# Kernel optimization log

Measured on AMD Instinct MI355X. Metric: run time of the kernel, lower is better.

Reference implementation:

```python
import jax, jax.numpy as jnp
import numpy as np

MANIFOLD_DIM = 256
EPS = 1e-8

def quaternion_normalize(q):
    # q: (..., 4) -> unit quaternions
    return q / (jnp.linalg.norm(q, axis=-1, keepdims=True) + EPS)

def quaternion_mul(a, b):
    # Hamilton product, broadcasting over leading dims. a, b: (..., 4)
    aw, ax, ay, az = a[..., 0], a[..., 1], a[..., 2], a[..., 3]
    bw, bx, by, bz = b[..., 0], b[..., 1], b[..., 2], b[..., 3]
    return jnp.stack([
        aw * bw - ax * bx - ay * by - az * bz,
        aw * bx + ax * bw + ay * bz - az * by,
        aw * by - ax * bz + ay * bw + az * bx,
        aw * bz + ax * by - ay * bx + az * bw,
    ], axis=-1)

def compute_berry_phase(path):
    # path: (B, N, 4). gamma = 2*acos(Re(q0*q1*...*q_{N-1}*q0))
    path = quaternion_normalize(path)
    # ordered product via log-depth parallel scan (quaternion mul is associative)
    prod_all = jax.lax.associative_scan(quaternion_mul, path, axis=1)[:, -1]  # (B, 4)
    prod = quaternion_mul(prod_all, path[:, 0])
    return 2.0 * jnp.arccos(jnp.clip(prod[..., 0], -1.0, 1.0))  # (B,)

def holomorphic_audit(q_state):
    # torch.gradient(t)[0] == gradient along dim 0 (batch axis), unit spacing.
    # dw+dx+dy+dz == gradient of the component-sum (linearity of gradient).
    df = jnp.abs(jnp.gradient(q_state.sum(axis=-1), axis=0))  # (B, N)
    res = jnp.mean(df)
    return res < 0.05, res

def _to_quaternion(x):
    B = x.shape[0]
    return x.reshape(B, -1, 4)

def setup_inputs() -> dict:
    key = jax.random.key(0)
    ks = jax.random.split(key, 9)
    B, HW, L, G, D = 8, 4096, 8192, 4096, MANIFOLD_DIM
    s = 0.05  # keep latents small so Berry product stays numerically tame
    return {
        "vision_data": jax.random.normal(ks[0], (B, HW, 3), jnp.float32),
        "text_data": jax.random.normal(ks[1], (B, L, 1), jnp.float32),
        "genomic_data": jax.random.normal(ks[2], (B, G, 4), jnp.float32),
        "Wv": jax.random.normal(ks[3], (3, D), jnp.float32) * s,
        "bv": jax.random.normal(ks[4], (D,), jnp.float32) * s,
        "Wt": jax.random.normal(ks[5], (1, D), jnp.float32) * s,
        "bt": jax.random.normal(ks[6], (D,), jnp.float32) * s,
        "Wg": jax.random.normal(ks[7], (4, D), jnp.float32) * s,
        "bg": jax.random.normal(ks[8], (D,), jnp.float32) * s,
    }

def reference(vision_data, text_data, genomic_data, Wv, bv, Wt, bt, Wg, bg):
    v_lat = vision_data @ Wv + bv      # (B, HW, 256)
    t_lat = text_data @ Wt + bt        # (B, L, 256)
    g_lat = genomic_data @ Wg + bg     # (B, G, 256)
    v_path = _to_quaternion(v_lat)     # (B, HW*64, 4)
    t_path = _to_quaternion(t_lat)
    g_path = _to_quaternion(g_lat)
    phi_v = compute_berry_phase(v_path)
    phi_t = compute_berry_phase(t_path)
    phi_g = compute_berry_phase(g_path)
    interference = jnp.abs(phi_v.mean() - phi_t.mean())
    genomic_invariant_score = jnp.exp(-jnp.abs(phi_g - interference))  # (B,)
    _, res_v = holomorphic_audit(v_path)
    _, res_t = holomorphic_audit(t_path)
    return genomic_invariant_score, interference, res_v, res_t
```

## Files before the change

kernel.cpp:

```cpp
#include <hip/hip_runtime.h>
#include <math.h>

#define BB 8
#define HW 4096
#define LTXT 8192
#define GG 4096
#define DD 256


struct QF { float w, x, y, z; };

__device__ __forceinline__ QF qmulf(const QF a, const QF b) {
    QF r;
    r.w = fmaf(a.w, b.w, -fmaf(a.x, b.x, fmaf(a.y, b.y, a.z * b.z)));
    r.x = fmaf(a.w, b.x, fmaf(a.x, b.w, fmaf(a.y, b.z, -(a.z * b.y))));
    r.y = fmaf(a.w, b.y, fmaf(a.y, b.w, fmaf(a.z, b.x, -(a.x * b.z))));
    r.z = fmaf(a.w, b.z, fmaf(a.x, b.y, fmaf(a.z, b.w, -(a.y * b.x))));
    return r;
}

__device__ __forceinline__ QF wave_ordered_prod(QF p, int lane) {
    #pragma unroll
    for (int s = 1; s < 64; s <<= 1) {
        QF o;
        o.w = __shfl_xor(p.w, s, 64);
        o.x = __shfl_xor(p.x, s, 64);
        o.y = __shfl_xor(p.y, s, 64);
        o.z = __shfl_xor(p.z, s, 64);
        const bool hi = (lane & s) != 0;
        QF a = hi ? o : p;
        QF b = hi ? p : o;
        p = qmulf(a, b);
    }
    return p;
}

template<int K, int BQ>
__device__ __forceinline__ void chain_block(
    const float* __restrict__ X, const float* __restrict__ W,
    const float* __restrict__ bias, int rowBase,
    float* __restrict__ out4, float* sprod)
{
    constexpr int V = K + 1;
    constexpr int NB = 64 / BQ;
    const int t = threadIdx.x;
    const int r = rowBase + t;
    float xv[K];
    #pragma unroll
    for (int k = 0; k < K; ++k) xv[k] = X[(size_t)r * K + k];

    float4 A[BQ * V], Bb[BQ * V];
    QF p = {1.0f, 0.0f, 0.0f, 0.0f};

    auto LOADB = [&](float4* dst, int bidx) {
        const float* bb = bias + 4 * (bidx * BQ);
        const float* wb = W + 4 * (bidx * BQ);
        #pragma unroll
        for (int j = 0; j < BQ; ++j) {
            dst[j * V + 0] = *(const float4*)(bb + 4 * j);
            #pragma unroll
            for (int k = 0; k < K; ++k)
                dst[j * V + 1 + k] = *(const float4*)(wb + k * DD + 4 * j);
        }
    };

    auto COMPUTE = [&](const float4* src, int bidx) {
        QF pb; float sb;
        #pragma unroll
        for (int j = 0; j < BQ; ++j) {
            const float4 b4 = src[j * V + 0];
            float l0 = b4.x, l1 = b4.y, l2 = b4.z, l3 = b4.w;
            #pragma unroll
            for (int k = 0; k < K; ++k) {
                const float4 w4 = src[j * V + 1 + k];
                l0 = fmaf(xv[k], w4.x, l0);
                l1 = fmaf(xv[k], w4.y, l1);
                l2 = fmaf(xv[k], w4.z, l2);
                l3 = fmaf(xv[k], w4.w, l3);
            }
            const float n = sqrtf(fmaf(l0, l0, fmaf(l1, l1, fmaf(l2, l2, l3 * l3))));
            QF q = { l0, l1, l2, l3 };
            if (j == 0) { pb = q; sb = n + 1e-8f; }
            else        { pb = qmulf(pb, q); sb *= (n + 1e-8f); }
        }
        const float inv = 1.0f / sb;
        QF pbn = { pb.w * inv, pb.x * inv, pb.y * inv, pb.z * inv };
        if (bidx == 0) p = pbn;
        else           p = qmulf(p, pbn);
    };

    LOADB(A, 0);
    for (int gg = 0; gg < NB / 2; ++gg) {
        LOADB(Bb, 2 * gg + 1);
        COMPUTE(A, 2 * gg);
        const int nb = (2 * gg + 2 < NB) ? (2 * gg + 2) : (NB - 1);
        LOADB(A, nb);
        COMPUTE(Bb, 2 * gg + 1);
    }

    const int lane = t & 63;
    p = wave_ordered_prod(p, lane);

    const int w = t >> 6;
    if (lane == 0) { sprod[w*4+0] = p.w; sprod[w*4+1] = p.x; sprod[w*4+2] = p.y; sprod[w*4+3] = p.z; }
    __syncthreads();
    if (t == 0) {
        QF pp = { sprod[0], sprod[1], sprod[2], sprod[3] };
        #pragma unroll
        for (int wv = 1; wv < 4; ++wv) {
            QF o = { sprod[wv*4+0], sprod[wv*4+1], sprod[wv*4+2], sprod[wv*4+3] };
            pp = qmulf(pp, o);
        }
        float4 outv = { pp.w, pp.x, pp.y, pp.z };
        *(float4*)out4 = outv;
    }
}

__global__ __launch_bounds__(256) void worker_kernel(
    const float* __restrict__ vis, const float* __restrict__ txt, const float* __restrict__ gen,
    const float* __restrict__ Wv, const float* __restrict__ bv,
    const float* __restrict__ Wt, const float* __restrict__ bt,
    const float* __restrict__ Wg, const float* __restrict__ bg,
    float* __restrict__ wsf, double* __restrict__ dws)
{
    __shared__ double sred[256];
    float* sprod = (float*)sred;

    const int t  = threadIdx.x;
    const int id = blockIdx.x;

    if (id < 128) {
        const int b = id >> 4, chunk = id & 15;
        chain_block<3, 4>(vis + (size_t)b * HW * 3, Wv, bv, chunk * 256,
                          wsf + (size_t)id * 4, sprod);
    } else if (id < 384) {
        const int i2 = id - 128;
        const int b = i2 >> 5, chunk = i2 & 31;
        chain_block<1, 8>(txt + (size_t)b * LTXT, Wt, bt, chunk * 256,
                          wsf + 512 + (size_t)i2 * 4, sprod);
    } else if (id < 512) {
        const int i2 = id - 384;
        const int b = i2 >> 4, chunk = i2 & 15;
        chain_block<4, 2>(gen + (size_t)b * GG * 4, Wg, bg, chunk * 256,
                          wsf + 1536 + (size_t)i2 * 4, sprod);
    } else if (id < 528) {
        const int aid = id - 512;
        const int r = aid * 256 + t;
        float gx[8], gy[8], gz[8];
        {
            float vx[8], vy[8], vz[8];
            #pragma unroll
            for (int b = 0; b < 8; ++b) {
                const size_t base = ((size_t)b * HW + r) * 3;
                vx[b] = vis[base]; vy[b] = vis[base+1]; vz[b] = vis[base+2];
            }
            #pragma unroll
            for (int b = 0; b < 8; ++b) {
                if (b == 0)      { gx[b] = vx[1]-vx[0];  gy[b] = vy[1]-vy[0];  gz[b] = vz[1]-vz[0]; }
                else if (b == 7) { gx[b] = vx[7]-vx[6];  gy[b] = vy[7]-vy[6];  gz[b] = vz[7]-vz[6]; }
                else             { gx[b] = (vx[b+1]-vx[b-1])*0.5f; gy[b] = (vy[b+1]-vy[b-1])*0.5f; gz[b] = (vz[b+1]-vz[b-1])*0.5f; }
            }
        }
        double acc = 0.0;
        #pragma unroll 4
        for (int i = 0; i < 64; ++i) {
            const float4 a0 = *(const float4*)(Wv + 4*i);
            const float4 a1 = *(const float4*)(Wv + DD + 4*i);
            const float4 a2 = *(const float4*)(Wv + 2*DD + 4*i);
            const float wq0 = a0.x + a0.y + a0.z + a0.w;
            const float wq1 = a1.x + a1.y + a1.z + a1.w;
            const float wq2 = a2.x + a2.y + a2.z + a2.w;
            float acc8 = 0.0f;
            #pragma unroll
            for (int b = 0; b < 8; ++b)
                acc8 += fabsf(fmaf(gx[b], wq0, fmaf(gy[b], wq1, gz[b] * wq2)));
            acc += (double)acc8;
        }
        sred[t] = acc;
        __syncthreads();
        for (int off = 128; off > 0; off >>= 1) {
            if (t < off) sred[t] += sred[t + off];
            __syncthreads();
        }
        if (t == 0) dws[aid] = sred[0];
    } else {
        const int aid = id - 528;
        const int l = aid * 256 + t;
        float tv[8];
        #pragma unroll
        for (int b = 0; b < 8; ++b) tv[b] = txt[(size_t)b * LTXT + l];
        double acc = 0.0;
        #pragma unroll
        for (int b = 0; b < 8; ++b) {
            float gb;
            if (b == 0)      gb = tv[1] - tv[0];
            else if (b == 7) gb = tv[7] - tv[6];
            else             gb = (tv[b+1] - tv[b-1]) * 0.5f;
            acc += (double)fabsf(gb);
        }
        sred[t] = acc;
        __syncthreads();
        for (int off = 128; off > 0; off >>= 1) {
            if (t < off) sred[t] += sred[t + off];
            __syncthreads();
        }
        if (t == 0) dws[16 + aid] = sred[0];
    }
}

__global__ __launch_bounds__(256) void finalize_kernel(
    const float* __restrict__ vis, const float* __restrict__ txt, const float* __restrict__ gen,
    const float* __restrict__ Wv, const float* __restrict__ bv,
    const float* __restrict__ Wt, const float* __restrict__ bt,
    const float* __restrict__ Wg, const float* __restrict__ bg,
    const float* __restrict__ wsf, const double* __restrict__ dws,
    float* __restrict__ out)
{
    __shared__ double sphi[24];
    __shared__ double sred[256];
    __shared__ double s_sumv, s_sumt, s_sumw;
    const int t = threadIdx.x;
    const int lane = t & 63, w = t >> 6;

    #pragma unroll
    for (int j = 0; j < 6; ++j) {
        const int pair = w * 6 + j;
        const int m = pair >> 3, b = pair & 7;
        const int nch = (m == 1) ? 32 : 16;
        const float* base = wsf + ((m == 0) ? 0 : (m == 1) ? 512 : 1536) + (size_t)b * nch * 4;
        QF p = { 1.0f, 0.0f, 0.0f, 0.0f };
        if (lane < nch) {
            const float4 c0 = *(const float4*)(base + lane * 4);
            p = { c0.x, c0.y, c0.z, c0.w };
        }
        p = wave_ordered_prod(p, lane);
        if (lane == 0) {
            float lat[4];
            if (m == 0) {
                const float x0 = vis[(size_t)b*HW*3], x1 = vis[(size_t)b*HW*3+1], x2 = vis[(size_t)b*HW*3+2];
                #pragma unroll
                for (int c = 0; c < 4; ++c)
                    lat[c] = fmaf(x0, Wv[c], fmaf(x1, Wv[DD+c], fmaf(x2, Wv[2*DD+c], bv[c])));
            } else if (m == 1) {
                const float x0 = txt[(size_t)b*LTXT];
                #pragma unroll
                for (int c = 0; c < 4; ++c) lat[c] = fmaf(x0, Wt[c], bt[c]);
            } else {
                const float x0 = gen[(size_t)b*GG*4], x1 = gen[(size_t)b*GG*4+1],
                            x2 = gen[(size_t)b*GG*4+2], x3 = gen[(size_t)b*GG*4+3];
                #pragma unroll
                for (int c = 0; c < 4; ++c)
                    lat[c] = fmaf(x0, Wg[c], fmaf(x1, Wg[DD+c], fmaf(x2, Wg[2*DD+c], fmaf(x3, Wg[3*DD+c], bg[c]))));
            }
            const float n = sqrtf(fmaf(lat[0], lat[0], fmaf(lat[1], lat[1], fmaf(lat[2], lat[2], lat[3] * lat[3]))));
            const float inv = 1.0f / (n + 1e-8f);
            QF q0 = { lat[0]*inv, lat[1]*inv, lat[2]*inv, lat[3]*inv };
            p = qmulf(p, q0);
            double ww = (double)p.w;
            if (ww > 1.0) ww = 1.0;
            if (ww < -1.0) ww = -1.0;
            sphi[pair] = 2.0 * acos(ww);
        }
    }
    __syncthreads();

    sred[t] = (t < 16) ? dws[t] : 0.0; __syncthreads();
    for (int off = 128; off > 0; off >>= 1) { if (t < off) sred[t] += sred[t+off]; __syncthreads(); }
    if (t == 0) s_sumv = sred[0];
    __syncthreads();

    sred[t] = (t < 32) ? dws[16 + t] : 0.0; __syncthreads();
    for (int off = 128; off > 0; off >>= 1) { if (t < off) sred[t] += sred[t+off]; __syncthreads(); }
    if (t == 0) s_sumt = sred[0];
    __syncthreads();

    double aw = 0.0;
    if (t < 64) {
        const int d0 = 4 * t;
        aw = (double)fabsf(Wt[d0] + Wt[d0+1] + Wt[d0+2] + Wt[d0+3]);
    }
    sred[t] = aw; __syncthreads();
    for (int off = 128; off > 0; off >>= 1) { if (t < off) sred[t] += sred[t+off]; __syncthreads(); }
    if (t == 0) s_sumw = sred[0];
    __syncthreads();

    if (t == 0) {
        double mv = 0.0, mt = 0.0;
        for (int b = 0; b < 8; ++b) { mv += sphi[b]; mt += sphi[8 + b]; }
        mv /= 8.0; mt /= 8.0;
        const double interf = fabs(mv - mt);
        for (int b = 0; b < 8; ++b)
            out[b] = (float)exp(-fabs(sphi[16 + b] - interf));
        out[8]  = (float)interf;
        out[9]  = (float)(s_sumv / 2097152.0);
        out[10] = (float)(s_sumt * s_sumw / 4194304.0);
    }
}

extern "C" void kernel_launch(void* const* d_in, const int* in_sizes, int n_in,
                              void* d_out, int out_size, void* d_ws, size_t ws_size,
                              hipStream_t stream) {
    (void)in_sizes; (void)n_in; (void)out_size; (void)ws_size;
    const float* vis = (const float*)d_in[0];
    const float* txt = (const float*)d_in[1];
    const float* gen = (const float*)d_in[2];
    const float* Wv  = (const float*)d_in[3];
    const float* bv  = (const float*)d_in[4];
    const float* Wt  = (const float*)d_in[5];
    const float* bt  = (const float*)d_in[6];
    const float* Wg  = (const float*)d_in[7];
    const float* bg  = (const float*)d_in[8];
    float*  wsf = (float*)d_ws;
    double* dws = (double*)((char*)d_ws + 65536);
    float*  out = (float*)d_out;

    hipLaunchKernelGGL(worker_kernel, dim3(560), dim3(256), 0, stream,
                       vis, txt, gen, Wv, bv, Wt, bt, Wg, bg, wsf, dws);
    hipLaunchKernelGGL(finalize_kernel, dim3(1), dim3(256), 0, stream,
                       vis, txt, gen, Wv, bv, Wt, bt, Wg, bg, wsf, dws, out);
}
```

Baseline: 35.31 us.

## Use single-wave blocks with two rows per thread and shuffle reductions

Worker blocks shrink from 256 threads to one 64-lane wave. Each thread now processes two consecutive rows, which amortizes the weight and bias loads across both chains. The LDS-based cross-wave quaternion product and the double tree reductions are replaced by wave shuffles with no __syncthreads, and the grid grows to 1216 blocks to keep coverage. This raises the chunk count the finalize kernel must combine and doubles per-thread register use, which may reduce occupancy.

```diff
diff --git a/kernel.cpp b/kernel.cpp
--- a/kernel.cpp
+++ b/kernel.cpp
@@ -36,28 +36,31 @@
 }
 
 template<int K, int BQ>
-__device__ __forceinline__ void chain_block(
+__device__ __forceinline__ void chain_block64(
     const float* __restrict__ X, const float* __restrict__ W,
-    const float* __restrict__ bias, int rowBase,
-    float* __restrict__ out4, float* sprod)
+    const float* __restrict__ bias, int rowBase, float* __restrict__ out4)
 {
     constexpr int V = K + 1;
     constexpr int NB = 64 / BQ;
     const int t = threadIdx.x;
-    const int r = rowBase + t;
-    float xv[K];
+    const int r0 = rowBase + 2 * t;
+
+    float xa[K], xb[K];
     #pragma unroll
-    for (int k = 0; k < K; ++k) xv[k] = X[(size_t)r * K + k];
-
-    float4 A[BQ * V], Bb[BQ * V];
-    QF p = {1.0f, 0.0f, 0.0f, 0.0f};
+    for (int k = 0; k < K; ++k) {
+        xa[k] = X[(size_t)r0 * K + k];
+        xb[k] = X[(size_t)(r0 + 1) * K + k];
+    }
+
+    float4 A[BQ * V], Bv[BQ * V];
+    QF pa = {1.0f, 0.0f, 0.0f, 0.0f}, pb = {1.0f, 0.0f, 0.0f, 0.0f};
 
     auto LOADB = [&](float4* dst, int bidx) {
         const float* bb = bias + 4 * (bidx * BQ);
         const float* wb = W + 4 * (bidx * BQ);
         #pragma unroll
         for (int j = 0; j < BQ; ++j) {
-            dst[j * V + 0] = *(const float4*)(bb + 4 * j);
+            dst[j * V] = *(const float4*)(bb + 4 * j);
             #pragma unroll
             for (int k = 0; k < K; ++k)
                 dst[j * V + 1 + k] = *(const float4*)(wb + k * DD + 4 * j);
@@ -65,87 +68,85 @@
     };
 
     auto COMPUTE = [&](const float4* src, int bidx) {
-        QF pb; float sb;
+        QF ga, gb; float sa, sb;
         #pragma unroll
         for (int j = 0; j < BQ; ++j) {
-            const float4 b4 = src[j * V + 0];
-            float l0 = b4.x, l1 = b4.y, l2 = b4.z, l3 = b4.w;
+            const float4 b4 = src[j * V];
+            float a0 = b4.x, a1 = b4.y, a2 = b4.z, a3 = b4.w;
+            float c0 = b4.x, c1 = b4.y, c2 = b4.z, c3 = b4.w;
             #pragma unroll
             for (int k = 0; k < K; ++k) {
                 const float4 w4 = src[j * V + 1 + k];
-                l0 = fmaf(xv[k], w4.x, l0);
-                l1 = fmaf(xv[k], w4.y, l1);
-                l2 = fmaf(xv[k], w4.z, l2);
-                l3 = fmaf(xv[k], w4.w, l3);
-            }
-            const float n = sqrtf(fmaf(l0, l0, fmaf(l1, l1, fmaf(l2, l2, l3 * l3))));
-            QF q = { l0, l1, l2, l3 };
-            if (j == 0) { pb = q; sb = n + 1e-8f; }
-            else        { pb = qmulf(pb, q); sb *= (n + 1e-8f); }
-        }
-        const float inv = 1.0f / sb;
-        QF pbn = { pb.w * inv, pb.x * inv, pb.y * inv, pb.z * inv };
-        if (bidx == 0) p = pbn;
-        else           p = qmulf(p, pbn);
+                a0 = fmaf(xa[k], w4.x, a0);
+                a1 = fmaf(xa[k], w4.y, a1);
+                a2 = fmaf(xa[k], w4.z, a2);
+                a3 = fmaf(xa[k], w4.w, a3);
+                c0 = fmaf(xb[k], w4.x, c0);
+                c1 = fmaf(xb[k], w4.y, c1);
+                c2 = fmaf(xb[k], w4.z, c2);
+                c3 = fmaf(xb[k], w4.w, c3);
+            }
+            const float na = sqrtf(fmaf(a0, a0, fmaf(a1, a1, fmaf(a2, a2, a3 * a3))));
+            const float nb = sqrtf(fmaf(c0, c0, fmaf(c1, c1, fmaf(c2, c2, c3 * c3))));
+            QF qa = { a0, a1, a2, a3 };
+            QF qb = { c0, c1, c2, c3 };
+            if (j == 0) { ga = qa; sa = na + 1e-8f; gb = qb; sb = nb + 1e-8f; }
+            else {
+                ga = qmulf(ga, qa); sa *= (na + 1e-8f);
+                gb = qmulf(gb, qb); sb *= (nb + 1e-8f);
+            }
+        }
+        const float ia = 1.0f / sa, ib = 1.0f / sb;
+        QF gan = { ga.w * ia, ga.x * ia, ga.y * ia, ga.z * ia };
+        QF gbn = { gb.w * ib, gb.x * ib, gb.y * ib, gb.z * ib };
+        if (bidx == 0) { pa = gan; pb = gbn; }
+        else           { pa = qmulf(pa, gan); pb = qmulf(pb, gbn); }
     };
 
     LOADB(A, 0);
     for (int gg = 0; gg < NB / 2; ++gg) {
-        LOADB(Bb, 2 * gg + 1);
+        LOADB(Bv, 2 * gg + 1);
         COMPUTE(A, 2 * gg);
-        const int nb = (2 * gg + 2 < NB) ? (2 * gg + 2) : (NB - 1);
-        LOADB(A, nb);
-        COMPUTE(Bb, 2 * gg + 1);
-    }
-
-    const int lane = t & 63;
-    p = wave_ordered_prod(p, lane);
-
-    const int w = t >> 6;
-    if (lane == 0) { sprod[w*4+0] = p.w; sprod[w*4+1] = p.x; sprod[w*4+2] = p.y; sprod[w*4+3] = p.z; }
-    __syncthreads();
+        const int nb2 = (2 * gg + 2 < NB) ? (2 * gg + 2) : (NB - 1);
+        LOADB(A, nb2);
+        COMPUTE(Bv, 2 * gg + 1);
+    }
+
+    QF p = qmulf(pa, pb);
+    p = wave_ordered_prod(p, t);
     if (t == 0) {
-        QF pp = { sprod[0], sprod[1], sprod[2], sprod[3] };
-        #pragma unroll
-        for (int wv = 1; wv < 4; ++wv) {
-            QF o = { sprod[wv*4+0], sprod[wv*4+1], sprod[wv*4+2], sprod[wv*4+3] };
-            pp = qmulf(pp, o);
-        }
-        float4 outv = { pp.w, pp.x, pp.y, pp.z };
-        *(float4*)out4 = outv;
-    }
-}
-
-__global__ __launch_bounds__(256) void worker_kernel(
+        float4 o = { p.w, p.x, p.y, p.z };
+        *(float4*)out4 = o;
+    }
+}
+
+__global__ __launch_bounds__(64) void worker_kernel(
     const float* __restrict__ vis, const float* __restrict__ txt, const float* __restrict__ gen,
     const float* __restrict__ Wv, const float* __restrict__ bv,
     const float* __restrict__ Wt, const float* __restrict__ bt,
     const float* __restrict__ Wg, const float* __restrict__ bg,
     float* __restrict__ wsf, double* __restrict__ dws)
 {
-    __shared__ double sred[256];
-    float* sprod = (float*)sred;
-
     const int t  = threadIdx.x;
     const int id = blockIdx.x;
 
-    if (id < 128) {
-        const int b = id >> 4, chunk = id & 15;
-        chain_block<3, 4>(vis + (size_t)b * HW * 3, Wv, bv, chunk * 256,
-                          wsf + (size_t)id * 4, sprod);
-    } else if (id < 384) {
-        const int i2 = id - 128;
+    if (id < 256) {
+        const int b = id >> 5, chunk = id & 31;
+        chain_block64<3, 4>(vis + (size_t)b * HW * 3, Wv, bv, chunk * 128,
+                            wsf + (size_t)id * 4);
+    } else if (id < 768) {
+        const int i2 = id - 256;
+        const int b = i2 >> 6, chunk = i2 & 63;
+        chain_block64<1, 8>(txt + (size_t)b * LTXT, Wt, bt, chunk * 128,
+                            wsf + 1024 + (size_t)i2 * 4);
+    } else if (id < 1024) {
+        const int i2 = id - 768;
         const int b = i2 >> 5, chunk = i2 & 31;
-        chain_block<1, 8>(txt + (size_t)b * LTXT, Wt, bt, chunk * 256,
-                          wsf + 512 + (size_t)i2 * 4, sprod);
-    } else if (id < 512) {
-        const int i2 = id - 384;
-        const int b = i2 >> 4, chunk = i2 & 15;
-        chain_block<4, 2>(gen + (size_t)b * GG * 4, Wg, bg, chunk * 256,
-                          wsf + 1536 + (size_t)i2 * 4, sprod);
-    } else if (id < 528) {
-        const int aid = id - 512;
-        const int r = aid * 256 + t;
+        chain_block64<4, 2>(gen + (size_t)b * GG * 4, Wg, bg, chunk * 128,
+                            wsf + 3072 + (size_t)i2 * 4);
+    } else if (id < 1088) {
+        const int aid = id - 1024;
+        const int r = aid * 64 + t;
         float gx[8], gy[8], gz[8];
         {
             float vx[8], vy[8], vz[8];
@@ -176,16 +177,12 @@
                 acc8 += fabsf(fmaf(gx[b], wq0, fmaf(gy[b], wq1, gz[b] * wq2)));
             acc += (double)acc8;
         }
-        sred[t] = acc;
-        __syncthreads();
-        for (int off = 128; off > 0; off >>= 1) {
-            if (t < off) sred[t] += sred[t + off];
-            __syncthreads();
-        }
-        if (t == 0) dws[aid] = sred[0];
+        #pragma unroll
+        for (int s = 32; s > 0; s >>= 1) acc += __shfl_down(acc, s, 64);
+        if (t == 0) dws[aid] = acc;
     } else {
-        const int aid = id - 528;
-        const int l = aid * 256 + t;
+        const int aid = id - 1088;
+        const int l = aid * 64 + t;
         float tv[8];
         #pragma unroll
         for (int b = 0; b < 8; ++b) tv[b] = txt[(size_t)b * LTXT + l];
@@ -198,13 +195,9 @@
             else             gb = (tv[b+1] - tv[b-1]) * 0.5f;
             acc += (double)fabsf(gb);
         }
-        sred[t] = acc;
-        __syncthreads();
-        for (int off = 128; off > 0; off >>= 1) {
-            if (t < off) sred[t] += sred[t + off];
-            __syncthreads();
-        }
-        if (t == 0) dws[16 + aid] = sred[0];
+        #pragma unroll
+        for (int s = 32; s > 0; s >>= 1) acc += __shfl_down(acc, s, 64);
+        if (t == 0) dws[64 + aid] = acc;
     }
 }
 
@@ -226,8 +219,8 @@
     for (int j = 0; j < 6; ++j) {
         const int pair = w * 6 + j;
         const int m = pair >> 3, b = pair & 7;
-        const int nch = (m == 1) ? 32 : 16;
-        const float* base = wsf + ((m == 0) ? 0 : (m == 1) ? 512 : 1536) + (size_t)b * nch * 4;
+        const int nch = (m == 1) ? 64 : 32;
+        const float* base = wsf + ((m == 0) ? 0 : (m == 1) ? 1024 : 3072) + (size_t)b * nch * 4;
         QF p = { 1.0f, 0.0f, 0.0f, 0.0f };
         if (lane < nch) {
             const float4 c0 = *(const float4*)(base + lane * 4);
@@ -264,12 +257,12 @@
     }
     __syncthreads();
 
-    sred[t] = (t < 16) ? dws[t] : 0.0; __syncthreads();
+    sred[t] = (t < 64) ? dws[t] : 0.0; __syncthreads();
     for (int off = 128; off > 0; off >>= 1) { if (t < off) sred[t] += sred[t+off]; __syncthreads(); }
     if (t == 0) s_sumv = sred[0];
     __syncthreads();
 
-    sred[t] = (t < 32) ? dws[16 + t] : 0.0; __syncthreads();
+    sred[t] = (t < 128) ? dws[64 + t] : 0.0; __syncthreads();
     for (int off = 128; off > 0; off >>= 1) { if (t < off) sred[t] += sred[t+off]; __syncthreads(); }
     if (t == 0) s_sumt = sred[0];
     __syncthreads();
@@ -314,7 +307,7 @@
     double* dws = (double*)((char*)d_ws + 65536);
     float*  out = (float*)d_out;
 
-    hipLaunchKernelGGL(worker_kernel, dim3(560), dim3(256), 0, stream,
+    hipLaunchKernelGGL(worker_kernel, dim3(1216), dim3(64), 0, stream,
                        vis, txt, gen, Wv, bv, Wt, bt, Wg, bg, wsf, dws);
     hipLaunchKernelGGL(finalize_kernel, dim3(1), dim3(256), 0, stream,
                        vis, txt, gen, Wv, bv, Wt, bt, Wg, bg, wsf, dws, out);
```

Measured after the change: 39.77 us. +12.6%, slower.
